# Optimization experiments

Measured on AMD Instinct MI355X. Metric: run time of the kernel, lower is better.

The kernel has to match this reference:

```python
import jax, jax.numpy as jnp
from jax import lax
import numpy as np

D_STATE = 16
D_CONV = 4
GROUPS = 4
TOKEN = 8


def group_norm(x, w, b, groups, eps=1e-5):
    # x: [B, C, H, W]; torch GroupNorm semantics
    B, C, H, W = x.shape
    xg = x.reshape(B, groups, C // groups, H, W)
    mu = xg.mean(axis=(2, 3, 4), keepdims=True)
    var = ((xg - mu) ** 2).mean(axis=(2, 3, 4), keepdims=True)
    xg = (xg - mu) / jnp.sqrt(var + eps)
    return xg.reshape(B, C, H, W) * w[None, :, None, None] + b[None, :, None, None]


def mamba_fwd(x, in_w, conv_w, conv_b, xproj_w, dt_w, dt_b, A_log, D, out_w):
    # x: [B, L, d_model]. Faithful mamba_ssm Mamba forward (no biases on in/out proj).
    Bsz, L, _ = x.shape
    d_inner = in_w.shape[0] // 2
    dt_rank = dt_w.shape[1]
    xz = x @ in_w.T                                   # [B, L, 2*d_inner]
    xi, z = jnp.split(xz, 2, axis=-1)
    # causal depthwise conv1d (kernel D_CONV) + SiLU
    xc = lax.conv_general_dilated(
        xi.transpose(0, 2, 1), conv_w, window_strides=(1,),
        padding=[(D_CONV - 1, 0)], dimension_numbers=("NCH", "OIH", "NCH"),
        feature_group_count=d_inner)
    xc = jax.nn.silu(xc + conv_b[None, :, None]).transpose(0, 2, 1)  # [B, L, d_inner]
    xdb = xc @ xproj_w.T                               # [B, L, dt_rank + 2*d_state]
    dt, Bm, Cm = jnp.split(xdb, [dt_rank, dt_rank + D_STATE], axis=-1)
    dt = jax.nn.softplus(dt @ dt_w.T + dt_b)           # [B, L, d_inner]
    A = -jnp.exp(A_log)                                # [d_inner, d_state]
    dA = jnp.exp(dt[..., None] * A)                    # [B, L, d_inner, d_state]
    dBx = dt[..., None] * Bm[:, :, None, :] * xc[..., None]

    def step(h, inp):
        dA_t, dBx_t, C_t = inp                         # [B,di,ds],[B,di,ds],[B,ds]
        h = dA_t * h + dBx_t
        y = jnp.einsum('bds,bs->bd', h, C_t)
        return h, y

    h0 = jnp.zeros((Bsz, d_inner, D_STATE), dtype=x.dtype)
    _, ys = lax.scan(step, h0, (dA.transpose(1, 0, 2, 3),
                                dBx.transpose(1, 0, 2, 3),
                                Cm.transpose(1, 0, 2)))
    y = ys.transpose(1, 0, 2) + xc * D                 # skip term D*x
    y = y * jax.nn.silu(z)
    return y @ out_w.T


def setup_inputs() -> dict:
    key = jax.random.key(0)
    ks = iter(jax.random.split(key, 48))

    def rn(shape, s=0.02):
        return jax.random.normal(next(ks), shape, dtype=jnp.float32) * s

    B, C, H, W = 4, 64, 64, 64
    inp = {"x": jax.random.normal(next(ks), (B, C, H, W), dtype=jnp.float32)}

    def mamba_params(prefix, d_model):
        d_inner = 2 * d_model
        dt_rank = -(-d_model // 16)
        inp[prefix + "_in_w"] = rn((2 * d_inner, d_model))
        inp[prefix + "_conv_w"] = rn((d_inner, 1, D_CONV))
        inp[prefix + "_conv_b"] = rn((d_inner,))
        inp[prefix + "_xproj_w"] = rn((dt_rank + 2 * D_STATE, d_inner))
        inp[prefix + "_dt_w"] = rn((d_inner, dt_rank))
        inp[prefix + "_dt_b"] = rn((d_inner,)) + 0.5
        inp[prefix + "_A_log"] = jnp.log(jnp.tile(jnp.arange(1, D_STATE + 1, dtype=jnp.float32), (d_inner, 1)))
        inp[prefix + "_D"] = jnp.ones((d_inner,), jnp.float32)
        inp[prefix + "_out_w"] = rn((d_model, d_inner))

    mamba_params("spa", C)
    mamba_params("spe", -(-C // TOKEN))  # group_channel_num = ceil(64/8) = 8
    inp["spa_gn_w"] = jnp.ones((C,), jnp.float32)
    inp["spa_gn_b"] = jnp.zeros((C,), jnp.float32)
    inp["spe_gn_w"] = jnp.ones((C,), jnp.float32)
    inp["spe_gn_b"] = jnp.zeros((C,), jnp.float32)
    inp["att_w"] = jnp.full((2,), 0.5, jnp.float32)
    return inp


def reference(x,
              spa_in_w, spa_conv_w, spa_conv_b, spa_xproj_w, spa_dt_w, spa_dt_b,
              spa_A_log, spa_D, spa_out_w,
              spe_in_w, spe_conv_w, spe_conv_b, spe_xproj_w, spe_dt_w, spe_dt_b,
              spe_A_log, spe_D, spe_out_w,
              spa_gn_w, spa_gn_b, spe_gn_w, spe_gn_b, att_w):
    B, C, H, W = x.shape
    gcn = -(-C // TOKEN)  # C == TOKEN*gcn here, so no padding path is taken

    # --- SpaMamba: flatten all pixels into one sequence [1, B*H*W, C] ---
    xs = x.transpose(0, 2, 3, 1).reshape(1, -1, C)
    ys = mamba_fwd(xs, spa_in_w, spa_conv_w, spa_conv_b, spa_xproj_w,
                   spa_dt_w, spa_dt_b, spa_A_log, spa_D, spa_out_w)
    ys = ys.reshape(B, H, W, C).transpose(0, 3, 1, 2)
    spa = jax.nn.silu(group_norm(ys, spa_gn_w, spa_gn_b, GROUPS)) + x

    # --- SpeMamba: per-pixel spectral tokens [B*H*W, TOKEN, gcn] ---
    xe = x.transpose(0, 2, 3, 1).reshape(B * H * W, TOKEN, gcn)
    ye = mamba_fwd(xe, spe_in_w, spe_conv_w, spe_conv_b, spe_xproj_w,
                   spe_dt_w, spe_dt_b, spe_A_log, spe_D, spe_out_w)
    ye = ye.reshape(B, H, W, C).transpose(0, 3, 1, 2)
    spe = x + jax.nn.silu(group_norm(ye, spe_gn_w, spe_gn_b, GROUPS))

    w = jax.nn.softmax(att_w)
    return spa * w[0] + spe * w[1] + x
```

## Files before the change

kernel.cpp:

```cpp
#include <hip/hip_runtime.h>

__device__ __forceinline__ float siluf(float x){ return x / (1.f + __expf(-x)); }
__device__ __forceinline__ float softplusf(float x){
    return fmaxf(x, 0.f) + __logf(1.f + __expf(-fabsf(x)));
}
#if __has_builtin(__builtin_amdgcn_exp2f)
__device__ __forceinline__ float fexp2(float x){ return __builtin_amdgcn_exp2f(x); }
#else
__device__ __forceinline__ float fexp2(float x){ return exp2f(x); }
#endif

__global__ void __launch_bounds__(256) k_xpose(const float* __restrict__ x, float* __restrict__ xs){
    __shared__ float t[64][65];
    int blk = blockIdx.x;
    int b = blk >> 6;
    int hw0 = (blk & 63) << 6;
    int tid = threadIdx.x;
    if (blk == 0 && tid < 192) xs[tid] = 0.f;
    const float* xb = x + b*262144 + hw0;
    #pragma unroll
    for (int it = 0; it < 16; ++it){
        int idx = it*256 + tid;
        t[idx>>6][idx&63] = xb[(idx>>6)*4096 + (idx&63)];
    }
    __syncthreads();
    float* xsb = xs + 192 + (size_t)(b*4096 + hw0)*64;
    #pragma unroll
    for (int it = 0; it < 16; ++it){
        int idx = it*256 + tid;
        xsb[(idx>>6)*64 + (idx&63)] = t[idx&63][idx>>6];
    }
}

__global__ void __launch_bounds__(256) k_inproj_conv(const float* __restrict__ xs,
        const float* __restrict__ in_w, const float* __restrict__ cw, const float* __restrict__ cb,
        float* __restrict__ xc, float* __restrict__ zb){
    int tid = threadIdx.x;
    int l0 = blockIdx.x * 8;
    float wr[64];
    const float4* w4 = (const float4*)(in_w + tid*64);
    #pragma unroll
    for (int k = 0; k < 16; ++k){
        float4 v = w4[k];
        wr[4*k]=v.x; wr[4*k+1]=v.y; wr[4*k+2]=v.z; wr[4*k+3]=v.w;
    }
    if (tid < 128){
        float acc[11];
        #pragma unroll
        for (int r = 0; r < 11; ++r) acc[r] = 0.f;
        const float4* xr = ((const float4*)xs) + (size_t)l0*16;
        #pragma unroll
        for (int k = 0; k < 16; ++k){
            #pragma unroll
            for (int r = 0; r < 11; ++r){
                float4 v = xr[r*16 + k];
                acc[r] = fmaf(v.x, wr[4*k],   acc[r]);
                acc[r] = fmaf(v.y, wr[4*k+1], acc[r]);
                acc[r] = fmaf(v.z, wr[4*k+2], acc[r]);
                acc[r] = fmaf(v.w, wr[4*k+3], acc[r]);
            }
        }
        float cw0 = cw[tid*4+0], cw1 = cw[tid*4+1], cw2 = cw[tid*4+2], cw3 = cw[tid*4+3];
        float cbd = cb[tid];
        #pragma unroll
        for (int r = 0; r < 8; ++r){
            float a = fmaf(cw0, acc[r],   cbd);
            a = fmaf(cw1, acc[r+1], a);
            a = fmaf(cw2, acc[r+2], a);
            a = fmaf(cw3, acc[r+3], a);
            xc[(size_t)(l0+r)*128 + tid] = siluf(a);
        }
    } else {
        float acc[8];
        #pragma unroll
        for (int r = 0; r < 8; ++r) acc[r] = 0.f;
        const float4* xr = ((const float4*)(xs + 192)) + (size_t)l0*16;
        #pragma unroll
        for (int k = 0; k < 16; ++k){
            #pragma unroll
            for (int r = 0; r < 8; ++r){
                float4 v = xr[r*16 + k];
                acc[r] = fmaf(v.x, wr[4*k],   acc[r]);
                acc[r] = fmaf(v.y, wr[4*k+1], acc[r]);
                acc[r] = fmaf(v.z, wr[4*k+2], acc[r]);
                acc[r] = fmaf(v.w, wr[4*k+3], acc[r]);
            }
        }
        int dz = tid - 128;
        #pragma unroll
        for (int r = 0; r < 8; ++r) zb[(size_t)(l0+r)*128 + dz] = acc[r];
    }
}

__global__ void __launch_bounds__(256) k_scan_p1(const float* __restrict__ xc,
        const float* __restrict__ xpw, const float* __restrict__ dtw, const float* __restrict__ dtb,
        const float* __restrict__ A_log, float* __restrict__ Pb, float* __restrict__ Qb){
    __shared__ float sxc[32*128];
    __shared__ float sbm[32*16];
    __shared__ __align__(16) float dtr[32][4];
    const int tid = threadIdx.x;
    const int ch = blockIdx.x;
    {
        const float4* src = (const float4*)(xc + (size_t)ch*4096);
        float4* dst = (float4*)sxc;
        #pragma unroll
        for (int u = 0; u < 4; ++u) dst[u*256 + tid] = src[u*256 + tid];
    }
    __syncthreads();
    {
        int j = tid & 63, tg = tid >> 6;
        if (j < 20){
            const float4* w4  = (const float4*)(xpw + j*128);
            const float4* xc4 = (const float4*)sxc + tg*256;
            float acc[8];
            #pragma unroll
            for (int r = 0; r < 8; ++r) acc[r] = 0.f;
            #pragma unroll 8
            for (int k = 0; k < 32; ++k){
                float4 w = w4[k];
                #pragma unroll
                for (int r = 0; r < 8; ++r){
                    float4 v = xc4[r*32 + k];
                    acc[r] = fmaf(v.x, w.x, acc[r]);
                    acc[r] = fmaf(v.y, w.y, acc[r]);
                    acc[r] = fmaf(v.z, w.z, acc[r]);
                    acc[r] = fmaf(v.w, w.w, acc[r]);
                }
            }
            if (j < 4){
                #pragma unroll
                for (int r = 0; r < 8; ++r) dtr[tg*8+r][j] = acc[r];
            } else {
                #pragma unroll
                for (int r = 0; r < 8; ++r) sbm[(tg*8+r)*16 + (j-4)] = acc[r];
            }
        }
    }
    __syncthreads();
    const int d  = tid & 127;
    const int sh = tid >> 7;
    float A8[8];
    {
        const float4* al4 = (const float4*)(A_log + d*16 + sh*8);
        float4 v0 = al4[0], v1 = al4[1];
        A8[0]=-__expf(v0.x)*1.44269504f; A8[1]=-__expf(v0.y)*1.44269504f;
        A8[2]=-__expf(v0.z)*1.44269504f; A8[3]=-__expf(v0.w)*1.44269504f;
        A8[4]=-__expf(v1.x)*1.44269504f; A8[5]=-__expf(v1.y)*1.44269504f;
        A8[6]=-__expf(v1.z)*1.44269504f; A8[7]=-__expf(v1.w)*1.44269504f;
    }
    float4 dw = *(const float4*)(dtw + d*4);
    float dbd = dtb[d];
    float P[8], Q[8];
    #pragma unroll
    for (int s = 0; s < 8; ++s){ P[s] = 1.f; Q[s] = 0.f; }
    #pragma unroll 4
    for (int i = 0; i < 32; ++i){
        float4 dt4 = *(const float4*)dtr[i];
        float dv = dbd;
        dv = fmaf(dt4.x, dw.x, dv);
        dv = fmaf(dt4.y, dw.y, dv);
        dv = fmaf(dt4.z, dw.z, dv);
        dv = fmaf(dt4.w, dw.w, dv);
        float dt = softplusf(dv);
        float db = dt * sxc[i*128 + d];
        const float4* bmr = (const float4*)(sbm + i*16 + sh*8);
        float4 b0 = bmr[0], b1 = bmr[1];
        float bv[8] = {b0.x,b0.y,b0.z,b0.w,b1.x,b1.y,b1.z,b1.w};
        #pragma unroll
        for (int s = 0; s < 8; ++s){
            float a = fexp2(dt*A8[s]);
            P[s] *= a;
            Q[s] = fmaf(a, Q[s], db*bv[s]);
        }
    }
    float* Pp = Pb + (size_t)ch*2048 + d*16 + sh*8;
    float* Qp = Qb + (size_t)ch*2048 + d*16 + sh*8;
    ((float4*)Pp)[0] = make_float4(P[0],P[1],P[2],P[3]);
    ((float4*)Pp)[1] = make_float4(P[4],P[5],P[6],P[7]);
    ((float4*)Qp)[0] = make_float4(Q[0],Q[1],Q[2],Q[3]);
    ((float4*)Qp)[1] = make_float4(Q[4],Q[5],Q[6],Q[7]);
}

__global__ void __launch_bounds__(256) k_scan_p2a(const float* __restrict__ Pb,
        const float* __restrict__ Qb, float* __restrict__ Ps, float* __restrict__ Qs){
    int g = blockIdx.x*256 + threadIdx.x;
    int sup = g >> 11;
    int lane = g & 2047;
    float P = 1.f, Q = 0.f;
    for (int i = 0; i < 32; i += 8){
        float p[8], q[8];
        #pragma unroll
        for (int u = 0; u < 8; ++u){
            p[u] = Pb[(size_t)(sup*32+i+u)*2048 + lane];
            q[u] = Qb[(size_t)(sup*32+i+u)*2048 + lane];
        }
        #pragma unroll
        for (int u = 0; u < 8; ++u){
            P = p[u]*P;
            Q = fmaf(p[u], Q, q[u]);
        }
    }
    Ps[g] = P; Qs[g] = Q;
}

__global__ void __launch_bounds__(256) k_scan_p2b(const float* __restrict__ Ps,
        const float* __restrict__ Qs, float* __restrict__ Hsup){
    int lane = blockIdx.x*256 + threadIdx.x;
    float h = 0.f;
    float p[16], q[16];
    #pragma unroll
    for (int u = 0; u < 16; ++u){ p[u] = Ps[u*2048+lane]; q[u] = Qs[u*2048+lane]; }
    #pragma unroll
    for (int u = 0; u < 16; ++u){ Hsup[u*2048+lane] = h; h = fmaf(p[u], h, q[u]); }
}

__global__ void __launch_bounds__(256) k_scan_p2c(const float* __restrict__ Pb,
        const float* __restrict__ Qb, const float* __restrict__ Hsup, float* __restrict__ Hs){
    int g = blockIdx.x*256 + threadIdx.x;
    int sup = g >> 11;
    int lane = g & 2047;
    float h = Hsup[(size_t)sup*2048 + lane];
    for (int i = 0; i < 32; i += 8){
        float p[8], q[8];
        #pragma unroll
        for (int u = 0; u < 8; ++u){
            p[u] = Pb[(size_t)(sup*32+i+u)*2048 + lane];
            q[u] = Qb[(size_t)(sup*32+i+u)*2048 + lane];
        }
        #pragma unroll
        for (int u = 0; u < 8; ++u){
            Hs[(size_t)(sup*32+i+u)*2048 + lane] = h;
            h = fmaf(p[u], h, q[u]);
        }
    }
}

__global__ void __launch_bounds__(256) k_scan_p3(const float* __restrict__ xc,
        const float* __restrict__ zb, const float* __restrict__ xpw, const float* __restrict__ dtw,
        const float* __restrict__ dtb, const float* __restrict__ A_log, const float* __restrict__ Dv,
        const float* __restrict__ Hs, float* __restrict__ yg){
    __shared__ float sxc[32*128];
    __shared__ float ypl[2][32*128];
    __shared__ float sbm[32*16];
    __shared__ float scm[32*16];
    __shared__ __align__(16) float dtr[32][4];
    const int tid = threadIdx.x;
    const int ch = blockIdx.x;
    {
        const float4* src = (const float4*)(xc + (size_t)ch*4096);
        float4* dst = (float4*)sxc;
        #pragma unroll
        for (int u = 0; u < 4; ++u) dst[u*256 + tid] = src[u*256 + tid];
    }
    __syncthreads();
    {
        int j = tid & 63, tg = tid >> 6;
        if (j < 36){
            const float4* w4  = (const float4*)(xpw + j*128);
            const float4* xc4 = (const float4*)sxc + tg*256;
            float acc[8];
            #pragma unroll
            for (int r = 0; r < 8; ++r) acc[r] = 0.f;
            #pragma unroll 8
            for (int k = 0; k < 32; ++k){
                float4 w = w4[k];
                #pragma unroll
                for (int r = 0; r < 8; ++r){
                    float4 v = xc4[r*32 + k];
                    acc[r] = fmaf(v.x, w.x, acc[r]);
                    acc[r] = fmaf(v.y, w.y, acc[r]);
                    acc[r] = fmaf(v.z, w.z, acc[r]);
                    acc[r] = fmaf(v.w, w.w, acc[r]);
                }
            }
            if (j < 4){
                #pragma unroll
                for (int r = 0; r < 8; ++r) dtr[tg*8+r][j] = acc[r];
            } else if (j < 20){
                #pragma unroll
                for (int r = 0; r < 8; ++r) sbm[(tg*8+r)*16 + (j-4)] = acc[r];
            } else {
                #pragma unroll
                for (int r = 0; r < 8; ++r) scm[(tg*8+r)*16 + (j-20)] = acc[r];
            }
        }
    }
    __syncthreads();
    const int d  = tid & 127;
    const int sh = tid >> 7;
    float A8[8], h[8];
    {
        const float4* al4 = (const float4*)(A_log + d*16 + sh*8);
        float4 v0 = al4[0], v1 = al4[1];
        A8[0]=-__expf(v0.x)*1.44269504f; A8[1]=-__expf(v0.y)*1.44269504f;
        A8[2]=-__expf(v0.z)*1.44269504f; A8[3]=-__expf(v0.w)*1.44269504f;
        A8[4]=-__expf(v1.x)*1.44269504f; A8[5]=-__expf(v1.y)*1.44269504f;
        A8[6]=-__expf(v1.z)*1.44269504f; A8[7]=-__expf(v1.w)*1.44269504f;
        const float4* h4 = (const float4*)(Hs + (size_t)ch*2048 + d*16 + sh*8);
        float4 h0 = h4[0], h1 = h4[1];
        h[0]=h0.x; h[1]=h0.y; h[2]=h0.z; h[3]=h0.w;
        h[4]=h1.x; h[5]=h1.y; h[6]=h1.z; h[7]=h1.w;
    }
    float4 dw = *(const float4*)(dtw + d*4);
    float dbd = dtb[d];
    #pragma unroll 4
    for (int i = 0; i < 32; ++i){
        float4 dt4 = *(const float4*)dtr[i];
        float dv = dbd;
        dv = fmaf(dt4.x, dw.x, dv);
        dv = fmaf(dt4.y, dw.y, dv);
        dv = fmaf(dt4.z, dw.z, dv);
        dv = fmaf(dt4.w, dw.w, dv);
        float dt = softplusf(dv);
        float db = dt * sxc[i*128 + d];
        const float4* bmr = (const float4*)(sbm + i*16 + sh*8);
        const float4* cmr = (const float4*)(scm + i*16 + sh*8);
        float4 b0 = bmr[0], b1 = bmr[1];
        float4 c0 = cmr[0], c1 = cmr[1];
        float bv[8] = {b0.x,b0.y,b0.z,b0.w,b1.x,b1.y,b1.z,b1.w};
        float cv[8] = {c0.x,c0.y,c0.z,c0.w,c1.x,c1.y,c1.z,c1.w};
        float yp = 0.f;
        #pragma unroll
        for (int s = 0; s < 8; ++s){
            float a = fexp2(dt*A8[s]);
            h[s] = fmaf(a, h[s], db*bv[s]);
            yp = fmaf(h[s], cv[s], yp);
        }
        ypl[sh][i*128 + d] = yp;
    }
    __syncthreads();
    #pragma unroll
    for (int it = 0; it < 16; ++it){
        int idx = it*256 + tid;
        int i = idx >> 7, dd = idx & 127;
        float yp = ypl[0][i*128+dd] + ypl[1][i*128+dd];
        float xcd = sxc[i*128+dd];
        float zv = zb[(size_t)ch*4096 + idx];
        yg[(size_t)ch*4096 + idx] = (yp + xcd*Dv[dd]) * siluf(zv);
    }
}

__global__ void __launch_bounds__(256) k_spa_outproj(const float* __restrict__ yg,
        const float* __restrict__ ow, float* __restrict__ ys){
    __shared__ float part[16][64];
    int tid = threadIdx.x;
    int c  = tid & 63;
    int kh = (tid >> 6) & 1;
    int rg = tid >> 7;
    int l0 = blockIdx.x*16 + rg*8;
    float wr[64];
    const float4* w4 = (const float4*)(ow + c*128 + kh*64);
    #pragma unroll
    for (int k = 0; k < 16; ++k){
        float4 v = w4[k];
        wr[4*k]=v.x; wr[4*k+1]=v.y; wr[4*k+2]=v.z; wr[4*k+3]=v.w;
    }
    float acc[8];
    #pragma unroll
    for (int r = 0; r < 8; ++r) acc[r] = 0.f;
    const float4* yr = (const float4*)(yg + (size_t)l0*128 + kh*64);
    #pragma unroll
    for (int k = 0; k < 16; ++k){
        #pragma unroll
        for (int r = 0; r < 8; ++r){
            float4 v = yr[r*32 + k];
            acc[r] = fmaf(v.x, wr[4*k],   acc[r]);
            acc[r] = fmaf(v.y, wr[4*k+1], acc[r]);
            acc[r] = fmaf(v.z, wr[4*k+2], acc[r]);
            acc[r] = fmaf(v.w, wr[4*k+3], acc[r]);
        }
    }
    if (kh == 1){
        #pragma unroll
        for (int r = 0; r < 8; ++r) part[rg*8+r][c] = acc[r];
    }
    __syncthreads();
    if (kh == 0){
        #pragma unroll
        for (int r = 0; r < 8; ++r)
            ys[(size_t)(l0+r)*64 + c] = acc[r] + part[rg*8+r][c];
    }
}

__global__ void __launch_bounds__(256) k_spe(
        const float* __restrict__ x,
        const float* __restrict__ in_w, const float* __restrict__ cw, const float* __restrict__ cb,
        const float* __restrict__ xpw, const float* __restrict__ dtw, const float* __restrict__ dtb,
        const float* __restrict__ A_log, const float* __restrict__ Dv, const float* __restrict__ ow,
        float* __restrict__ ye)
{
    __shared__ float xe[64][17];
    __shared__ float xcl[8][16][17];
    __shared__ float bml[8][16][17];
    __shared__ float cml[8][16][17];
    __shared__ float dtl[8][17];
    __shared__ float yl[8][16][17];

    const int tid = threadIdx.x;
    const int pix = tid >> 4;
    const int d   = tid & 15;
    const int p0  = blockIdx.x * 16;
    const int b   = p0 >> 12;
    const int hw0 = p0 & 4095;

    const float* xb = x + b*262144 + hw0;
    #pragma unroll
    for (int it = 0; it < 4; ++it){
        int idx = it*256 + tid;
        xe[idx>>4][idx&15] = xb[(idx>>4)*4096 + (idx&15)];
    }
    __syncthreads();

    float wi[8], wz[8];
    #pragma unroll
    for (int g = 0; g < 8; ++g){ wi[g] = in_w[d*8+g]; wz[g] = in_w[(16+d)*8+g]; }
    float xi[8], zz[8];
    #pragma unroll
    for (int t = 0; t < 8; ++t){
        float ai = 0.f, az = 0.f;
        #pragma unroll
        for (int g = 0; g < 8; ++g){
            float v = xe[t*8+g][pix];
            ai = fmaf(v, wi[g], ai);
            az = fmaf(v, wz[g], az);
        }
        xi[t] = ai; zz[t] = az;
    }
    float c0 = cw[d*4+0], c1 = cw[d*4+1], c2 = cw[d*4+2], c3 = cw[d*4+3];
    float cbd = cb[d];
    float xcr[8];
    #pragma unroll
    for (int t = 0; t < 8; ++t){
        float a = fmaf(c3, xi[t], cbd);
        if (t >= 1) a = fmaf(c2, xi[t-1], a);
        if (t >= 2) a = fmaf(c1, xi[t-2], a);
        if (t >= 3) a = fmaf(c0, xi[t-3], a);
        xcr[t] = siluf(a);
        xcl[t][d][pix] = xcr[t];
    }
    __syncthreads();

    {
        const float* wr = xpw + d*16;
        #pragma unroll
        for (int t = 0; t < 8; ++t){
            float acc = 0.f;
            #pragma unroll
            for (int k = 0; k < 16; ++k) acc = fmaf(xcl[t][k][pix], wr[k], acc);
            if (d == 0) dtl[t][pix] = acc;
            else bml[t][d-1][pix] = acc;
        }
    }
    {
        const float* wr = xpw + (17+d)*16;
        #pragma unroll
        for (int t = 0; t < 8; ++t){
            float acc = 0.f;
            #pragma unroll
            for (int k = 0; k < 16; ++k) acc = fmaf(xcl[t][k][pix], wr[k], acc);
            cml[t][d][pix] = acc;
        }
    }
    if (d == 15){
        const float* wr = xpw + 16*16;
        #pragma unroll
        for (int t = 0; t < 8; ++t){
            float acc = 0.f;
            #pragma unroll
            for (int k = 0; k < 16; ++k) acc = fmaf(xcl[t][k][pix], wr[k], acc);
            bml[t][15][pix] = acc;
        }
    }
    __syncthreads();

    float A16[16];
    #pragma unroll
    for (int s = 0; s < 16; ++s) A16[s] = -__expf(A_log[d*16+s]) * 1.44269504f;
    float dwd = dtw[d], dbd = dtb[d], Dd = Dv[d];
    float h[16];
    #pragma unroll
    for (int s = 0; s < 16; ++s) h[s] = 0.f;
    #pragma unroll
    for (int t = 0; t < 8; ++t){
        float dtd = softplusf(fmaf(dtl[t][pix], dwd, dbd));
        float db = dtd * xcr[t];
        float yp = 0.f;
        #pragma unroll
        for (int s = 0; s < 16; ++s){
            float a = fexp2(dtd*A16[s]);
            h[s] = fmaf(a, h[s], db*bml[t][s][pix]);
            yp = fmaf(h[s], cml[t][s][pix], yp);
        }
        yl[t][d][pix] = (yp + xcr[t]*Dd) * siluf(zz[t]);
    }
    __syncthreads();

    int t = d >> 1, m0 = (d & 1)*4;
    float acc[4];
    #pragma unroll
    for (int mm = 0; mm < 4; ++mm){
        const float* wr = ow + (m0+mm)*16;
        float a = 0.f;
        #pragma unroll
        for (int k = 0; k < 16; ++k) a = fmaf(yl[t][k][pix], wr[k], a);
        acc[mm] = a;
    }
    float4 o; o.x=acc[0]; o.y=acc[1]; o.z=acc[2]; o.w=acc[3];
    *(float4*)(ye + (size_t)(p0+pix)*64 + t*8 + m0) = o;
}

__global__ void __launch_bounds__(256) k_stats(const float* __restrict__ ys,
        const float* __restrict__ ye, float* __restrict__ partial){
    int blk = blockIdx.x;
    int t = blk >> 6;
    int b = (blk >> 4) & 3;
    int slice = blk & 15;
    const float* src = (t == 0) ? ys : ye;
    int tid = threadIdx.x;
    int c4 = tid & 15;
    int rowoff = tid >> 4;
    float s = 0.f, ss = 0.f;
    const float* base = src + ((size_t)(b*4096 + slice*256))*64 + c4*4;
    #pragma unroll
    for (int it = 0; it < 16; ++it){
        float4 v = *(const float4*)(base + (size_t)(it*16 + rowoff)*64);
        s  += v.x+v.y+v.z+v.w;
        ss += v.x*v.x+v.y*v.y+v.z*v.z+v.w*v.w;
    }
    s += __shfl_xor(s, 1);  ss += __shfl_xor(ss, 1);
    s += __shfl_xor(s, 2);  ss += __shfl_xor(ss, 2);
    s += __shfl_xor(s, 16); ss += __shfl_xor(ss, 16);
    s += __shfl_xor(s, 32); ss += __shfl_xor(ss, 32);
    __shared__ float sb[2][4][4];
    int wv = tid >> 6;
    int lane = tid & 63;
    int g = (lane >> 2) & 3;
    if ((lane & 51) == 0){ sb[0][wv][g] = s; sb[1][wv][g] = ss; }
    __syncthreads();
    if (tid < 4){
        float st  = sb[0][0][tid]+sb[0][1][tid]+sb[0][2][tid]+sb[0][3][tid];
        float sst = sb[1][0][tid]+sb[1][1][tid]+sb[1][2][tid]+sb[1][3][tid];
        int gi = t*16 + b*4 + tid;
        partial[gi*32 + slice*2]     = st;
        partial[gi*32 + slice*2 + 1] = sst;
    }
}

__global__ void __launch_bounds__(256) k_final(const float* __restrict__ x,
        const float* __restrict__ ys, const float* __restrict__ ye,
        const float* __restrict__ partial,
        const float* __restrict__ gsw, const float* __restrict__ gsb,
        const float* __restrict__ gew, const float* __restrict__ geb,
        const float* __restrict__ attw, float* __restrict__ out){
    __shared__ float st[16];
    __shared__ float tys[32][65];
    __shared__ float tye[32][65];
    int tid = threadIdx.x;
    int b   = blockIdx.x >> 7;
    int hw0 = (blockIdx.x & 127) << 5;
    if (tid < 128){
        int combo = tid >> 4;
        int sl = tid & 15;
        int gi = (combo >> 2)*16 + b*4 + (combo & 3);
        float s  = partial[gi*32 + sl*2];
        float ss = partial[gi*32 + sl*2 + 1];
        s += __shfl_down(s, 8, 16); ss += __shfl_down(ss, 8, 16);
        s += __shfl_down(s, 4, 16); ss += __shfl_down(ss, 4, 16);
        s += __shfl_down(s, 2, 16); ss += __shfl_down(ss, 2, 16);
        s += __shfl_down(s, 1, 16); ss += __shfl_down(ss, 1, 16);
        if (sl == 0){
            float m = s * (1.f/65536.f);
            float v = ss * (1.f/65536.f) - m*m;
            st[combo*2]   = m;
            st[combo*2+1] = rsqrtf(v + 1e-5f);
        }
    }
    const float* ysb = ys + ((size_t)(b*4096 + hw0))*64;
    const float* yeb = ye + ((size_t)(b*4096 + hw0))*64;
    #pragma unroll
    for (int it = 0; it < 8; ++it){
        int idx = it*256 + tid;
        tys[idx>>6][idx&63] = ysb[idx];
        tye[idx>>6][idx&63] = yeb[idx];
    }
    __syncthreads();
    float a0 = attw[0], a1 = attw[1];
    float mx = fmaxf(a0, a1);
    float e0 = __expf(a0-mx), e1 = __expf(a1-mx);
    float inv = 1.f/(e0+e1);
    float w0 = e0*inv, w1 = e1*inv;
    #pragma unroll
    for (int it = 0; it < 8; ++it){
        int idx = it*256 + tid;
        int c = idx >> 5, hwi = idx & 31;
        int g = c >> 4;
        size_t gx = ((size_t)(b*64 + c))*4096 + hw0 + hwi;
        float xv = x[gx];
        float ns = (tys[hwi][c] - st[g*2])     * st[g*2+1]     * gsw[c] + gsb[c];
        float ne = (tye[hwi][c] - st[8+g*2])   * st[8+g*2+1]   * gew[c] + geb[c];
        out[gx] = w0*(siluf(ns)+xv) + w1*(xv+siluf(ne)) + xv;
    }
}

#define OFF_XS 0u
#define OFF_XC 1048832u
#define OFF_Z  3145984u
#define OFF_PB 5243136u
#define OFF_QB 6291712u
#define OFF_HS 7340288u
#define OFF_PS 8388864u
#define OFF_QS 8421632u
#define OFF_HU 8454400u
#define OFF_SP 8487168u

extern "C" void kernel_launch(void* const* d_in, const int* in_sizes, int n_in,
                              void* d_out, int out_size, void* d_ws, size_t ws_size,
                              hipStream_t stream) {
    const float* x           = (const float*)d_in[0];
    const float* spa_in_w    = (const float*)d_in[1];
    const float* spa_conv_w  = (const float*)d_in[2];
    const float* spa_conv_b  = (const float*)d_in[3];
    const float* spa_xproj_w = (const float*)d_in[4];
    const float* spa_dt_w    = (const float*)d_in[5];
    const float* spa_dt_b    = (const float*)d_in[6];
    const float* spa_A_log   = (const float*)d_in[7];
    const float* spa_D       = (const float*)d_in[8];
    const float* spa_out_w   = (const float*)d_in[9];
    const float* spe_in_w    = (const float*)d_in[10];
    const float* spe_conv_w  = (const float*)d_in[11];
    const float* spe_conv_b  = (const float*)d_in[12];
    const float* spe_xproj_w = (const float*)d_in[13];
    const float* spe_dt_w    = (const float*)d_in[14];
    const float* spe_dt_b    = (const float*)d_in[15];
    const float* spe_A_log   = (const float*)d_in[16];
    const float* spe_D       = (const float*)d_in[17];
    const float* spe_out_w   = (const float*)d_in[18];
    const float* spa_gn_w    = (const float*)d_in[19];
    const float* spa_gn_b    = (const float*)d_in[20];
    const float* spe_gn_w    = (const float*)d_in[21];
    const float* spe_gn_b    = (const float*)d_in[22];
    const float* att_w       = (const float*)d_in[23];

    float* ws  = (float*)d_ws;
    float* xs  = ws + OFF_XS;
    float* xc  = ws + OFF_XC;
    float* zb  = ws + OFF_Z;
    float* Pb  = ws + OFF_PB;
    float* Qb  = ws + OFF_QB;
    float* Hs  = ws + OFF_HS;
    float* Ps  = ws + OFF_PS;
    float* Qs  = ws + OFF_QS;
    float* Hu  = ws + OFF_HU;
    float* sp  = ws + OFF_SP;
    float* yg  = ws + OFF_PB;
    float* ysb = ws + OFF_XS;
    float* yeb = ws + OFF_Z;
    float* out = (float*)d_out;

    k_xpose      <<<256,  256, 0, stream>>>(x, xs);
    k_inproj_conv<<<2048, 256, 0, stream>>>(xs, spa_in_w, spa_conv_w, spa_conv_b, xc, zb);
    k_scan_p1    <<<512,  256, 0, stream>>>(xc, spa_xproj_w, spa_dt_w, spa_dt_b, spa_A_log, Pb, Qb);
    k_scan_p2a   <<<128,  256, 0, stream>>>(Pb, Qb, Ps, Qs);
    k_scan_p2b   <<<8,    256, 0, stream>>>(Ps, Qs, Hu);
    k_scan_p2c   <<<128,  256, 0, stream>>>(Pb, Qb, Hu, Hs);
    k_scan_p3    <<<512,  256, 0, stream>>>(xc, zb, spa_xproj_w, spa_dt_w, spa_dt_b,
                                            spa_A_log, spa_D, Hs, yg);
    k_spa_outproj<<<1024, 256, 0, stream>>>(yg, spa_out_w, ysb);
    k_spe        <<<1024, 256, 0, stream>>>(x, spe_in_w, spe_conv_w, spe_conv_b, spe_xproj_w,
                                            spe_dt_w, spe_dt_b, spe_A_log, spe_D, spe_out_w, yeb);
    k_stats      <<<128,  256, 0, stream>>>(ysb, yeb, sp);
    k_final      <<<512,  256, 0, stream>>>(x, ysb, yeb, sp, spa_gn_w, spa_gn_b,
                                            spe_gn_w, spe_gn_b, att_w, out);
}
```

Baseline: 143.2 us.

## Fold scan carry propagation into p3 and fuse GroupNorm stats into producers

Removes the k_scan_p2b and k_scan_p2c kernels. Each k_scan_p3 block now recomputes its own starting state by serially combining the super-chunk aggregates and the chunk P/Q values before it, and keeps the result in shared memory. This drops the Hs buffer write and read and two launches, at the cost of redundant serial work that grows with chunk index, up to 15+31 steps per block. It also removes k_stats by having k_spa_outproj and k_spe emit per-block partial sums and sums of squares, which k_final then reduces.

Result: slower. 149.3 us (+4.2%).

```diff
diff --git a/kernel.cpp b/kernel.cpp
--- a/kernel.cpp
+++ b/kernel.cpp
@@ -181,7 +181,7 @@
     ((float4*)Qp)[1] = make_float4(Q[4],Q[5],Q[6],Q[7]);
 }
 
-__global__ void __launch_bounds__(256) k_scan_p2a(const float* __restrict__ Pb,
+__global__ void __launch_bounds__(256) k_scan_p2(const float* __restrict__ Pb,
         const float* __restrict__ Qb, float* __restrict__ Ps, float* __restrict__ Qs){
     int g = blockIdx.x*256 + threadIdx.x;
     int sup = g >> 11;
@@ -203,47 +203,17 @@
     Ps[g] = P; Qs[g] = Q;
 }
 
-__global__ void __launch_bounds__(256) k_scan_p2b(const float* __restrict__ Ps,
-        const float* __restrict__ Qs, float* __restrict__ Hsup){
-    int lane = blockIdx.x*256 + threadIdx.x;
-    float h = 0.f;
-    float p[16], q[16];
-    #pragma unroll
-    for (int u = 0; u < 16; ++u){ p[u] = Ps[u*2048+lane]; q[u] = Qs[u*2048+lane]; }
-    #pragma unroll
-    for (int u = 0; u < 16; ++u){ Hsup[u*2048+lane] = h; h = fmaf(p[u], h, q[u]); }
-}
-
-__global__ void __launch_bounds__(256) k_scan_p2c(const float* __restrict__ Pb,
-        const float* __restrict__ Qb, const float* __restrict__ Hsup, float* __restrict__ Hs){
-    int g = blockIdx.x*256 + threadIdx.x;
-    int sup = g >> 11;
-    int lane = g & 2047;
-    float h = Hsup[(size_t)sup*2048 + lane];
-    for (int i = 0; i < 32; i += 8){
-        float p[8], q[8];
-        #pragma unroll
-        for (int u = 0; u < 8; ++u){
-            p[u] = Pb[(size_t)(sup*32+i+u)*2048 + lane];
-            q[u] = Qb[(size_t)(sup*32+i+u)*2048 + lane];
-        }
-        #pragma unroll
-        for (int u = 0; u < 8; ++u){
-            Hs[(size_t)(sup*32+i+u)*2048 + lane] = h;
-            h = fmaf(p[u], h, q[u]);
-        }
-    }
-}
-
 __global__ void __launch_bounds__(256) k_scan_p3(const float* __restrict__ xc,
         const float* __restrict__ zb, const float* __restrict__ xpw, const float* __restrict__ dtw,
         const float* __restrict__ dtb, const float* __restrict__ A_log, const float* __restrict__ Dv,
-        const float* __restrict__ Hs, float* __restrict__ yg){
+        const float* __restrict__ Pb, const float* __restrict__ Qb,
+        const float* __restrict__ Ps, const float* __restrict__ Qs, float* __restrict__ yg){
     __shared__ float sxc[32*128];
     __shared__ float ypl[2][32*128];
     __shared__ float sbm[32*16];
     __shared__ float scm[32*16];
     __shared__ __align__(16) float dtr[32][4];
+    __shared__ float hbuf[2048];
     const int tid = threadIdx.x;
     const int ch = blockIdx.x;
     {
@@ -251,6 +221,33 @@
         float4* dst = (float4*)sxc;
         #pragma unroll
         for (int u = 0; u < 4; ++u) dst[u*256 + tid] = src[u*256 + tid];
+    }
+    {
+        const int sup = ch >> 5;
+        const int lb  = ch & 31;
+        float4 hA = make_float4(0.f,0.f,0.f,0.f), hB = hA;
+        const float4* Ps4 = (const float4*)Ps + tid*2;
+        const float4* Qs4 = (const float4*)Qs + tid*2;
+        for (int u = 0; u < sup; ++u){
+            float4 pA = Ps4[u*512], pB = Ps4[u*512+1];
+            float4 qA = Qs4[u*512], qB = Qs4[u*512+1];
+            hA.x = fmaf(pA.x, hA.x, qA.x); hA.y = fmaf(pA.y, hA.y, qA.y);
+            hA.z = fmaf(pA.z, hA.z, qA.z); hA.w = fmaf(pA.w, hA.w, qA.w);
+            hB.x = fmaf(pB.x, hB.x, qB.x); hB.y = fmaf(pB.y, hB.y, qB.y);
+            hB.z = fmaf(pB.z, hB.z, qB.z); hB.w = fmaf(pB.w, hB.w, qB.w);
+        }
+        const float4* Pb4 = (const float4*)Pb + (size_t)(ch & ~31)*512 + tid*2;
+        const float4* Qb4 = (const float4*)Qb + (size_t)(ch & ~31)*512 + tid*2;
+        for (int j = 0; j < lb; ++j){
+            float4 pA = Pb4[j*512], pB = Pb4[j*512+1];
+            float4 qA = Qb4[j*512], qB = Qb4[j*512+1];
+            hA.x = fmaf(pA.x, hA.x, qA.x); hA.y = fmaf(pA.y, hA.y, qA.y);
+            hA.z = fmaf(pA.z, hA.z, qA.z); hA.w = fmaf(pA.w, hA.w, qA.w);
+            hB.x = fmaf(pB.x, hB.x, qB.x); hB.y = fmaf(pB.y, hB.y, qB.y);
+            hB.z = fmaf(pB.z, hB.z, qB.z); hB.w = fmaf(pB.w, hB.w, qB.w);
+        }
+        ((float4*)hbuf)[tid*2]   = hA;
+        ((float4*)hbuf)[tid*2+1] = hB;
     }
     __syncthreads();
     {
@@ -296,7 +293,7 @@
         A8[2]=-__expf(v0.z)*1.44269504f; A8[3]=-__expf(v0.w)*1.44269504f;
         A8[4]=-__expf(v1.x)*1.44269504f; A8[5]=-__expf(v1.y)*1.44269504f;
         A8[6]=-__expf(v1.z)*1.44269504f; A8[7]=-__expf(v1.w)*1.44269504f;
-        const float4* h4 = (const float4*)(Hs + (size_t)ch*2048 + d*16 + sh*8);
+        const float4* h4 = (const float4*)hbuf + d*4 + sh*2;
         float4 h0 = h4[0], h1 = h4[1];
         h[0]=h0.x; h[1]=h0.y; h[2]=h0.z; h[3]=h0.w;
         h[4]=h1.x; h[5]=h1.y; h[6]=h1.z; h[7]=h1.w;
@@ -341,8 +338,9 @@
 }
 
 __global__ void __launch_bounds__(256) k_spa_outproj(const float* __restrict__ yg,
-        const float* __restrict__ ow, float* __restrict__ ys){
+        const float* __restrict__ ow, float* __restrict__ ys, float* __restrict__ sp){
     __shared__ float part[16][64];
+    __shared__ float pg[2][2][4];
     int tid = threadIdx.x;
     int c  = tid & 63;
     int kh = (tid >> 6) & 1;
@@ -376,9 +374,26 @@
     }
     __syncthreads();
     if (kh == 0){
-        #pragma unroll
-        for (int r = 0; r < 8; ++r)
-            ys[(size_t)(l0+r)*64 + c] = acc[r] + part[rg*8+r][c];
+        float s = 0.f, ss = 0.f;
+        #pragma unroll
+        for (int r = 0; r < 8; ++r){
+            float v = acc[r] + part[rg*8+r][c];
+            ys[(size_t)(l0+r)*64 + c] = v;
+            s += v; ss += v*v;
+        }
+        s += __shfl_xor(s,1); ss += __shfl_xor(ss,1);
+        s += __shfl_xor(s,2); ss += __shfl_xor(ss,2);
+        s += __shfl_xor(s,4); ss += __shfl_xor(ss,4);
+        s += __shfl_xor(s,8); ss += __shfl_xor(ss,8);
+        if ((c & 15) == 0){ pg[0][rg][c>>4] = s; pg[1][rg][c>>4] = ss; }
+    }
+    __syncthreads();
+    if (tid < 4){
+        int b = blockIdx.x >> 8, blk = blockIdx.x & 255;
+        float S  = pg[0][0][tid] + pg[0][1][tid];
+        float SS = pg[1][0][tid] + pg[1][1][tid];
+        float* dst = sp + (size_t)(((0*4 + b)*4 + tid)*256 + blk)*2;
+        dst[0] = S; dst[1] = SS;
     }
 }
 
@@ -387,7 +402,7 @@
         const float* __restrict__ in_w, const float* __restrict__ cw, const float* __restrict__ cb,
         const float* __restrict__ xpw, const float* __restrict__ dtw, const float* __restrict__ dtb,
         const float* __restrict__ A_log, const float* __restrict__ Dv, const float* __restrict__ ow,
-        float* __restrict__ ye)
+        float* __restrict__ ye, float* __restrict__ sp)
 {
     __shared__ float xe[64][17];
     __shared__ float xcl[8][16][17];
@@ -395,6 +410,7 @@
     __shared__ float cml[8][16][17];
     __shared__ float dtl[8][17];
     __shared__ float yl[8][16][17];
+    __shared__ float spg[2][4][4];
 
     const int tid = threadIdx.x;
     const int pix = tid >> 4;
@@ -507,48 +523,28 @@
     }
     float4 o; o.x=acc[0]; o.y=acc[1]; o.z=acc[2]; o.w=acc[3];
     *(float4*)(ye + (size_t)(p0+pix)*64 + t*8 + m0) = o;
-}
-
-__global__ void __launch_bounds__(256) k_stats(const float* __restrict__ ys,
-        const float* __restrict__ ye, float* __restrict__ partial){
-    int blk = blockIdx.x;
-    int t = blk >> 6;
-    int b = (blk >> 4) & 3;
-    int slice = blk & 15;
-    const float* src = (t == 0) ? ys : ye;
-    int tid = threadIdx.x;
-    int c4 = tid & 15;
-    int rowoff = tid >> 4;
-    float s = 0.f, ss = 0.f;
-    const float* base = src + ((size_t)(b*4096 + slice*256))*64 + c4*4;
-    #pragma unroll
-    for (int it = 0; it < 16; ++it){
-        float4 v = *(const float4*)(base + (size_t)(it*16 + rowoff)*64);
-        s  += v.x+v.y+v.z+v.w;
-        ss += v.x*v.x+v.y*v.y+v.z*v.z+v.w*v.w;
-    }
-    s += __shfl_xor(s, 1);  ss += __shfl_xor(ss, 1);
-    s += __shfl_xor(s, 2);  ss += __shfl_xor(ss, 2);
-    s += __shfl_xor(s, 16); ss += __shfl_xor(ss, 16);
-    s += __shfl_xor(s, 32); ss += __shfl_xor(ss, 32);
-    __shared__ float sb[2][4][4];
-    int wv = tid >> 6;
-    int lane = tid & 63;
-    int g = (lane >> 2) & 3;
-    if ((lane & 51) == 0){ sb[0][wv][g] = s; sb[1][wv][g] = ss; }
+
+    float s  = acc[0]+acc[1]+acc[2]+acc[3];
+    float ss = acc[0]*acc[0]+acc[1]*acc[1]+acc[2]*acc[2]+acc[3]*acc[3];
+    s += __shfl_xor(s,1);  ss += __shfl_xor(ss,1);
+    s += __shfl_xor(s,2);  ss += __shfl_xor(ss,2);
+    s += __shfl_xor(s,16); ss += __shfl_xor(ss,16);
+    s += __shfl_xor(s,32); ss += __shfl_xor(ss,32);
+    int lane = tid & 63, wv = tid >> 6;
+    if ((lane & 51) == 0){ spg[0][wv][(lane>>2)&3] = s; spg[1][wv][(lane>>2)&3] = ss; }
     __syncthreads();
     if (tid < 4){
-        float st  = sb[0][0][tid]+sb[0][1][tid]+sb[0][2][tid]+sb[0][3][tid];
-        float sst = sb[1][0][tid]+sb[1][1][tid]+sb[1][2][tid]+sb[1][3][tid];
-        int gi = t*16 + b*4 + tid;
-        partial[gi*32 + slice*2]     = st;
-        partial[gi*32 + slice*2 + 1] = sst;
+        int blk = blockIdx.x & 255;
+        float S  = spg[0][0][tid]+spg[0][1][tid]+spg[0][2][tid]+spg[0][3][tid];
+        float SS = spg[1][0][tid]+spg[1][1][tid]+spg[1][2][tid]+spg[1][3][tid];
+        float* dst = sp + (size_t)(((1*4 + b)*4 + tid)*256 + blk)*2;
+        dst[0] = S; dst[1] = SS;
     }
 }
 
 __global__ void __launch_bounds__(256) k_final(const float* __restrict__ x,
         const float* __restrict__ ys, const float* __restrict__ ye,
-        const float* __restrict__ partial,
+        const float* __restrict__ sp,
         const float* __restrict__ gsw, const float* __restrict__ gsb,
         const float* __restrict__ gew, const float* __restrict__ geb,
         const float* __restrict__ attw, float* __restrict__ out){
@@ -558,17 +554,20 @@
     int tid = threadIdx.x;
     int b   = blockIdx.x >> 7;
     int hw0 = (blockIdx.x & 127) << 5;
-    if (tid < 128){
-        int combo = tid >> 4;
-        int sl = tid & 15;
-        int gi = (combo >> 2)*16 + b*4 + (combo & 3);
-        float s  = partial[gi*32 + sl*2];
-        float ss = partial[gi*32 + sl*2 + 1];
-        s += __shfl_down(s, 8, 16); ss += __shfl_down(ss, 8, 16);
-        s += __shfl_down(s, 4, 16); ss += __shfl_down(ss, 4, 16);
-        s += __shfl_down(s, 2, 16); ss += __shfl_down(ss, 2, 16);
-        s += __shfl_down(s, 1, 16); ss += __shfl_down(ss, 1, 16);
-        if (sl == 0){
+    {
+        int combo = tid >> 5;
+        int j = tid & 31;
+        int t = combo >> 2, g = combo & 3;
+        const float4* bp = (const float4*)(sp + (size_t)((t*4+b)*4 + g)*512 + j*16);
+        float s = 0.f, ss = 0.f;
+        #pragma unroll
+        for (int k = 0; k < 4; ++k){ float4 v = bp[k]; s += v.x+v.z; ss += v.y+v.w; }
+        s += __shfl_xor(s,1);  ss += __shfl_xor(ss,1);
+        s += __shfl_xor(s,2);  ss += __shfl_xor(ss,2);
+        s += __shfl_xor(s,4);  ss += __shfl_xor(ss,4);
+        s += __shfl_xor(s,8);  ss += __shfl_xor(ss,8);
+        s += __shfl_xor(s,16); ss += __shfl_xor(ss,16);
+        if (j == 0){
             float m = s * (1.f/65536.f);
             float v = ss * (1.f/65536.f) - m*m;
             st[combo*2]   = m;
@@ -607,11 +606,10 @@
 #define OFF_Z  3145984u
 #define OFF_PB 5243136u
 #define OFF_QB 6291712u
-#define OFF_HS 7340288u
-#define OFF_PS 8388864u
-#define OFF_QS 8421632u
-#define OFF_HU 8454400u
-#define OFF_SP 8487168u
+#define OFF_YG 7340288u
+#define OFF_PS 9437440u
+#define OFF_QS 9470208u
+#define OFF_SP 9502976u
 
 extern "C" void kernel_launch(void* const* d_in, const int* in_sizes, int n_in,
                               void* d_out, int out_size, void* d_ws, size_t ws_size,
@@ -647,12 +645,10 @@
     float* zb  = ws + OFF_Z;
     float* Pb  = ws + OFF_PB;
     float* Qb  = ws + OFF_QB;
-    float* Hs  = ws + OFF_HS;
+    float* yg  = ws + OFF_YG;
     float* Ps  = ws + OFF_PS;
     float* Qs  = ws + OFF_QS;
-    float* Hu  = ws + OFF_HU;
     float* sp  = ws + OFF_SP;
-    float* yg  = ws + OFF_PB;
     float* ysb = ws + OFF_XS;
     float* yeb = ws + OFF_Z;
     float* out = (float*)d_out;
@@ -660,15 +656,13 @@
     k_xpose      <<<256,  256, 0, stream>>>(x, xs);
     k_inproj_conv<<<2048, 256, 0, stream>>>(xs, spa_in_w, spa_conv_w, spa_conv_b, xc, zb);
     k_scan_p1    <<<512,  256, 0, stream>>>(xc, spa_xproj_w, spa_dt_w, spa_dt_b, spa_A_log, Pb, Qb);
-    k_scan_p2a   <<<128,  256, 0, stream>>>(Pb, Qb, Ps, Qs);
-    k_scan_p2b   <<<8,    256, 0, stream>>>(Ps, Qs, Hu);
-    k_scan_p2c   <<<128,  256, 0, stream>>>(Pb, Qb, Hu, Hs);
+    k_scan_p2    <<<128,  256, 0, stream>>>(Pb, Qb, Ps, Qs);
     k_scan_p3    <<<512,  256, 0, stream>>>(xc, zb, spa_xproj_w, spa_dt_w, spa_dt_b,
-                                            spa_A_log, spa_D, Hs, yg);
-    k_spa_outproj<<<1024, 256, 0, stream>>>(yg, spa_out_w, ysb);
+                                            spa_A_log, spa_D, Pb, Qb, Ps, Qs, yg);
+    k_spa_outproj<<<1024, 256, 0, stream>>>(yg, spa_out_w, ysb, sp);
     k_spe        <<<1024, 256, 0, stream>>>(x, spe_in_w, spe_conv_w, spe_conv_b, spe_xproj_w,
-                                            spe_dt_w, spe_dt_b, spe_A_log, spe_D, spe_out_w, yeb);
-    k_stats      <<<128,  256, 0, stream>>>(ysb, yeb, sp);
+                                            spe_dt_w, spe_dt_b, spe_A_log, spe_D, spe_out_w,
+                                            yeb, sp);
     k_final      <<<512,  256, 0, stream>>>(x, ysb, yeb, sp, spa_gn_w, spa_gn_b,
                                             spe_gn_w, spe_gn_b, att_w, out);
 }
```
